# Performance work log

Hardware: AMD Instinct MI355X
Metric: run time of the kernel (lower is better)

The kernel has to match this reference:

```python
import jax, jax.numpy as jnp
import numpy as np

B, S, DIM = 2, 2048, 2048
H = 16
Q_LORA, KV_LORA = 512, 512
D_NOPE, D_ROPE, D_V = 128, 64, 128
D_QK = D_NOPE + D_ROPE  # 192
SCALE = D_QK ** -0.5
EPS = 1e-6


def rmsnorm(x, w):
    return x * jax.lax.rsqrt(jnp.mean(x * x, axis=-1, keepdims=True) + EPS) * w


def apply_rope(x, cos, sin):
    # x: [B, S, h, d] with d even; cos/sin: [S, d//2] (complex-pair rotation)
    xs = x.reshape(*x.shape[:-1], -1, 2)
    x0, x1 = xs[..., 0], xs[..., 1]
    c = cos[None, :, None, :]
    s = sin[None, :, None, :]
    out = jnp.stack([x0 * c - x1 * s, x0 * s + x1 * c], axis=-1)
    return out.reshape(x.shape)


def setup_inputs() -> dict:
    key = jax.random.key(0)
    ks = jax.random.split(key, 8)
    std = 0.02
    x = jax.random.normal(ks[0], (B, S, DIM), dtype=jnp.float32)
    wq_a_w = jax.random.normal(ks[1], (DIM, Q_LORA), dtype=jnp.float32) * std
    wq_a_b = jnp.zeros((Q_LORA,), dtype=jnp.float32)
    q_norm_w = jnp.ones((Q_LORA,), dtype=jnp.float32)
    wq_b_w = jax.random.normal(ks[2], (Q_LORA, H * D_QK), dtype=jnp.float32) * std
    wkv_a_w = jax.random.normal(ks[3], (DIM, KV_LORA + D_ROPE), dtype=jnp.float32) * std
    wkv_a_b = jnp.zeros((KV_LORA + D_ROPE,), dtype=jnp.float32)
    kv_norm_w = jnp.ones((KV_LORA,), dtype=jnp.float32)
    wkv_b_w = jax.random.normal(ks[4], (KV_LORA, H * (D_NOPE + D_V)), dtype=jnp.float32) * std
    wo_w = jax.random.normal(ks[5], (H * D_V, DIM), dtype=jnp.float32) * std
    # rotary table: freqs_cis[t, i] = exp(1j * t * 10000^{-2i/d})
    inv_freq = 1.0 / (10000.0 ** (np.arange(0, D_ROPE, 2, dtype=np.float32) / D_ROPE))
    t = np.arange(S, dtype=np.float32)
    ang = np.outer(t, inv_freq)  # [S, D_ROPE//2]
    freqs_cos = jnp.asarray(np.cos(ang), dtype=jnp.float32)
    freqs_sin = jnp.asarray(np.sin(ang), dtype=jnp.float32)
    # causal mask (prefill): 0 on/below diagonal, -1e9 above
    mask = jnp.where(jnp.arange(S)[:, None] >= jnp.arange(S)[None, :], 0.0, -1e9).astype(jnp.float32)
    return {"x": x, "wq_a_w": wq_a_w, "wq_a_b": wq_a_b, "q_norm_w": q_norm_w,
            "wq_b_w": wq_b_w, "wkv_a_w": wkv_a_w, "wkv_a_b": wkv_a_b,
            "kv_norm_w": kv_norm_w, "wkv_b_w": wkv_b_w, "wo_w": wo_w,
            "freqs_cos": freqs_cos, "freqs_sin": freqs_sin, "mask": mask,
            "start_pos": 0}


def reference(x, wq_a_w, wq_a_b, q_norm_w, wq_b_w, wkv_a_w, wkv_a_b,
              kv_norm_w, wkv_b_w, wo_w, freqs_cos, freqs_sin, mask, start_pos):
    bsz, seqlen, _ = x.shape
    # low-rank Q: wq_b(q_norm(wq_a(x)))
    q = rmsnorm(x @ wq_a_w + wq_a_b, q_norm_w) @ wq_b_w
    q = q.reshape(bsz, seqlen, H, D_QK)
    q_nope, q_pe = q[..., :D_NOPE], q[..., D_NOPE:]
    q_pe = apply_rope(q_pe, freqs_cos, freqs_sin)
    # low-rank KV
    kv_full = x @ wkv_a_w + wkv_a_b
    kv, k_pe = kv_full[..., :KV_LORA], kv_full[..., KV_LORA:]
    k_pe = apply_rope(k_pe[:, :, None, :], freqs_cos, freqs_sin)  # [B,S,1,D_ROPE]
    kv = rmsnorm(kv, kv_norm_w) @ wkv_b_w
    kv = kv.reshape(bsz, seqlen, H, D_NOPE + D_V)
    k_nope, v = kv[..., :D_NOPE], kv[..., D_NOPE:]
    k = jnp.concatenate([k_nope, jnp.broadcast_to(k_pe, (bsz, seqlen, H, D_ROPE))], axis=-1)
    # prefill (start_pos=0): cache[:, :end_pos] == freshly written k, v
    q = jnp.concatenate([q_nope, q_pe], axis=-1)
    scores = jnp.einsum('bshd,bthd->bsht', q, k) * SCALE
    scores = scores + mask[None, :, None, :]
    attn = jax.nn.softmax(scores.astype(jnp.float32), axis=-1).astype(q.dtype)
    out = jnp.einsum('bsht,bthd->bshd', attn, v)
    return out.reshape(bsz, seqlen, H * D_V) @ wo_w
```

## Files before the change

### kernel.cpp

```cpp
#include <hip/hip_runtime.h>
#include <hip/hip_bf16.h>

typedef unsigned short u16;
typedef unsigned int u32;
typedef __attribute__((ext_vector_type(8))) __bf16 bf16x8;
typedef __attribute__((ext_vector_type(4))) float f32x4;
typedef __attribute__((ext_vector_type(4))) u32 u32x4;
typedef __attribute__((ext_vector_type(2))) u32 u32x2;

#define S_LEN 2048
#define BF16_ONE 0x3F80u

__device__ __forceinline__ float b2f(u16 u) {
  union { unsigned u; float f; } v; v.u = ((unsigned)u) << 16; return v.f;
}
__device__ __forceinline__ u16 f2b(float f) {
  union { float f; unsigned u; } v; v.f = f;
  unsigned r = v.u + 0x7fffu + ((v.u >> 16) & 1u);
  return (u16)(r >> 16);
}
__device__ __forceinline__ u32 cvt_pk_bf16(float a, float b) {
  u32 r;
  asm("v_cvt_pk_bf16_f32 %0, %1, %2" : "=v"(r) : "v"(a), "v"(b));
  return r;
}

__device__ __forceinline__ void glds16(const u16* g, u16* l) {
  __builtin_amdgcn_global_load_lds((const __attribute__((address_space(1))) void*)g,
                                   (__attribute__((address_space(3))) void*)l, 16, 0, 0);
}

__device__ __forceinline__ bool probe_f32(const u16* p) { return p[0] != (u16)BF16_ONE; }

struct CvtDesc {
  const void* src[7];
  u16* dst[7];
  int cum[8];
};
__global__ __launch_bounds__(256) void cvt_batch(CvtDesc d, const u16* __restrict__ probe,
                                                 int total) {
  int i = blockIdx.x * 256 + threadIdx.x;
  if (i >= total) return;
  int t = 0;
#pragma unroll
  for (int k = 1; k < 7; ++k) t += (i >= d.cum[k]);
  int li = i - d.cum[t];
  if (probe_f32(probe)) {
    const float* s = (const float*)d.src[t] + (long)li * 8;
    u16 tmp[8];
#pragma unroll
    for (int j = 0; j < 8; ++j) tmp[j] = f2b(s[j]);
    *(u32x4*)(d.dst[t] + (long)li * 8) = *(const u32x4*)tmp;
  } else {
    *(u32x4*)(d.dst[t] + (long)li * 8) = ((const u32x4*)d.src[t])[li];
  }
}

struct TrDesc {
  const void* in[5];
  u16* out[5];
  int R[5], C[5];
  int tcum[6];
  float scale[5];
};
__global__ __launch_bounds__(256) void transpose_batch(TrDesc d,
                                                       const u16* __restrict__ probe) {
  __shared__ u16 tile[32][33];
  int bid = blockIdx.x;
  int t = 0;
#pragma unroll
  for (int k = 1; k < 5; ++k) t += (bid >= d.tcum[k]);
  int rem = bid - d.tcum[t];
  const int R = d.R[t], C = d.C[t];
  const int tilesX = C >> 5;
  const int bx = rem % tilesX, by = rem / tilesX;
  const int c0 = bx * 32, r0 = by * 32;
  const int tx = threadIdx.x, ty = threadIdx.y;
  const float sc = d.scale[t];
  if (probe_f32(probe)) {
    const float* inf = (const float*)d.in[t];
#pragma unroll
    for (int i = 0; i < 4; ++i)
      tile[ty + i * 8][tx] = f2b(inf[(long)(r0 + ty + i * 8) * C + c0 + tx] * sc);
  } else {
    const u16* inb = (const u16*)d.in[t];
#pragma unroll
    for (int i = 0; i < 4; ++i)
      tile[ty + i * 8][tx] = f2b(b2f(inb[(long)(r0 + ty + i * 8) * C + c0 + tx]) * sc);
  }
  __syncthreads();
  u16* outp = d.out[t];
#pragma unroll
  for (int i = 0; i < 4; ++i)
    outp[(long)(c0 + ty + i * 8) * R + r0 + tx] = tile[tx][ty + i * 8];
}

__global__ __launch_bounds__(256) void transpose_v(const u16* __restrict__ kvb,
                                                   u16* __restrict__ vt) {
  __shared__ u16 tile[32][33];
  int s0 = blockIdx.x * 32, d0 = blockIdx.y * 32, bh = blockIdx.z;
  int b = bh >> 4, h = bh & 15;
  int tx = threadIdx.x, ty = threadIdx.y;
#pragma unroll
  for (int i = 0; i < 4; ++i)
    tile[ty + i * 8][tx] =
        kvb[((long)b * S_LEN + s0 + ty + i * 8) * 4096 + h * 256 + 128 + d0 + tx];
  __syncthreads();
#pragma unroll
  for (int i = 0; i < 4; ++i)
    vt[((long)bh * 128 + d0 + ty + i * 8) * S_LEN + s0 + tx] = tile[tx][ty + i * 8];
}

template <int MT>
__global__ __launch_bounds__(256) void gemm_bt(const u16* __restrict__ A,
                                               const u16* __restrict__ Bt,
                                               const u16* __restrict__ bias,
                                               void* __restrict__ Cv,
                                               int M, int N, int K,
                                               const u16* __restrict__ oprobe) {
  constexpr int MI = MT / 32;
  __shared__ u16 As[2][MT * 32];
  __shared__ u16 Bs[2][128 * 32];
  const int tid = threadIdx.x;
  const int lane = tid & 63;
  const int w = tid >> 6;
  const int quad = lane >> 4;
  const int l16 = lane & 15;
  const int m0 = blockIdx.y * MT;
  const int n0 = blockIdx.x * 128;
  const int wm = (w >> 1) * (MT / 2);
  const int wn = (w & 1) * 64;

  const f32x4 zero = {0.f, 0.f, 0.f, 0.f};
  f32x4 acc[MI][4];
#pragma unroll
  for (int i = 0; i < MI; ++i)
#pragma unroll
    for (int j = 0; j < 4; ++j) acc[i][j] = zero;

  auto stage = [&](int k0, int buf) {
#pragma unroll
    for (int cc = 0; cc < MT * 4; cc += 256) {
      int j = cc + tid, ar = j >> 2, ak = ((j & 3) ^ (ar & 3)) * 8;
      glds16(A + (long)(m0 + ar) * K + k0 + ak, As[buf] + j * 8);
    }
#pragma unroll
    for (int cc = 0; cc < 512; cc += 256) {
      int j = cc + tid, br = j >> 2, bk = ((j & 3) ^ (br & 3)) * 8;
      int bn = n0 + br; if (bn > N - 1) bn = N - 1;
      glds16(Bt + (long)bn * K + k0 + bk, Bs[buf] + j * 8);
    }
  };

  const int nk = K >> 5;
  stage(0, 0);
  for (int t = 0; t < nk; ++t) {
    __syncthreads();
    if (t + 1 < nk) stage((t + 1) << 5, (t + 1) & 1);
    const u16* as = As[t & 1];
    const u16* bs = Bs[t & 1];
    bf16x8 af[MI], bfr[4];
#pragma unroll
    for (int mi = 0; mi < MI; ++mi)
      af[mi] = *(const bf16x8*)(as + (wm + mi * 16 + l16) * 32 +
                                ((quad ^ (l16 & 3)) * 8));
#pragma unroll
    for (int ni = 0; ni < 4; ++ni)
      bfr[ni] = *(const bf16x8*)(bs + (wn + ni * 16 + l16) * 32 +
                                 ((quad ^ (l16 & 3)) * 8));
#pragma unroll
    for (int mi = 0; mi < MI; ++mi)
#pragma unroll
      for (int ni = 0; ni < 4; ++ni)
        acc[mi][ni] = __builtin_amdgcn_mfma_f32_16x16x32_bf16(af[mi], bfr[ni],
                                                              acc[mi][ni], 0, 0, 0);
  }

  u16* C = (u16*)Cv;
  float* Cf = (float*)Cv;
  const bool of32 = oprobe && probe_f32(oprobe);
#pragma unroll
  for (int ni = 0; ni < 4; ++ni) {
    int col = n0 + wn + ni * 16 + l16;
    if (col >= N) continue;
    float bv = bias ? b2f(bias[col]) : 0.0f;
#pragma unroll
    for (int mi = 0; mi < MI; ++mi) {
      int row = m0 + wm + mi * 16 + quad * 4;
#pragma unroll
      for (int r = 0; r < 4; ++r) {
        float val = acc[mi][ni][r] + bv;
        if (of32) Cf[(long)(row + r) * N + col] = val;
        else      C[(long)(row + r) * N + col] = f2b(val);
      }
    }
  }
}

__global__ __launch_bounds__(256) void rmsnorm512(const u16* __restrict__ in, int in_stride,
                                                  const u16* __restrict__ w,
                                                  u16* __restrict__ out, int out_stride) {
  __shared__ float red[4];
  int row = blockIdx.x, tid = threadIdx.x;
  const u16* x = in + (long)row * in_stride;
  float v0 = b2f(x[tid]), v1 = b2f(x[tid + 256]);
  float ss = v0 * v0 + v1 * v1;
#pragma unroll
  for (int off = 1; off < 64; off <<= 1) ss += __shfl_xor(ss, off);
  if ((tid & 63) == 0) red[tid >> 6] = ss;
  __syncthreads();
  float tot = red[0] + red[1] + red[2] + red[3];
  float r = rsqrtf(tot * (1.0f / 512.0f) + 1e-6f);
  u16* y = out + (long)row * out_stride;
  y[tid] = f2b(v0 * r * b2f(w[tid]));
  y[tid + 256] = f2b(v1 * r * b2f(w[tid + 256]));
}

__global__ __launch_bounds__(256) void rope_q_kernel(u16* __restrict__ q,
                                                     const u16* __restrict__ fc,
                                                     const u16* __restrict__ fs) {
  int i = blockIdx.x * 256 + threadIdx.x;
  int pair = i & 31;
  int h = (i >> 5) & 15;
  int row = i >> 9;
  int pos = row & (S_LEN - 1);
  long base = (long)row * 3072 + h * 192 + 128 + pair * 2;
  float x0 = b2f(q[base]), x1 = b2f(q[base + 1]);
  float c = b2f(fc[pos * 32 + pair]), s = b2f(fs[pos * 32 + pair]);
  q[base] = f2b(x0 * c - x1 * s);
  q[base + 1] = f2b(x0 * s + x1 * c);
}

__global__ __launch_bounds__(256) void rope_k_kernel(const u16* __restrict__ qkva,
                                                     u16* __restrict__ kpe,
                                                     const u16* __restrict__ fc,
                                                     const u16* __restrict__ fs) {
  int i = blockIdx.x * 256 + threadIdx.x;
  int pair = i & 31;
  int row = i >> 5;
  int pos = row & (S_LEN - 1);
  long sb = (long)row * 1088 + 1024 + pair * 2;
  float x0 = b2f(qkva[sb]), x1 = b2f(qkva[sb + 1]);
  float c = b2f(fc[pos * 32 + pair]), s = b2f(fs[pos * 32 + pair]);
  kpe[(long)row * 64 + pair * 2] = f2b(x0 * c - x1 * s);
  kpe[(long)row * 64 + pair * 2 + 1] = f2b(x0 * s + x1 * c);
}

__global__ __launch_bounds__(512, 1) void mla_attn(const u16* __restrict__ q,
                                                   const u16* __restrict__ kvb,
                                                   const u16* __restrict__ vt,
                                                   const u16* __restrict__ kpe,
                                                   u16* __restrict__ o) {
  __shared__ u16 Ks[2][2][64 * 192];
  __shared__ u16 Vts[2][128 * 64];
  const int tid = threadIdx.x;
  const int w = tid >> 6;
  const int g = w >> 2;
  const int sw = w & 3;
  const int lane = tid & 63;
  const int quad = lane >> 4;
  const int l16 = lane & 15;
  const int bh = blockIdx.x;
  const int b = bh >> 4, h = bh & 15;
  const long rowbase = (long)b * S_LEN;
  const f32x4 zero = {0.f, 0.f, 0.f, 0.f};

  auto stage_k = [&](int t0s, u16* dst) {
#pragma unroll
    for (int tt = 0; tt < 3; ++tt) {
      int j = tt * 512 + tid;
      int r = j / 24, csw = j % 24;
      int c = csw ^ (r & 7);
      const u16* src = (c < 16)
                           ? (kvb + (rowbase + t0s + r) * 4096 + h * 256 + c * 8)
                           : (kpe + (rowbase + t0s + r) * 64 + (c - 16) * 8);
      glds16(src, dst + j * 8);
    }
  };
  auto stage_v = [&](int t0s, u16* dst) {
#pragma unroll
    for (int tt = 0; tt < 2; ++tt) {
      int j = tt * 512 + tid;
      int d = j >> 3, c = (j & 7) ^ (d & 7);
      glds16(vt + ((long)bh * 128 + d) * S_LEN + t0s + c * 8, dst + j * 8);
    }
  };

  const int srcA = (((quad & 1) << 1) | (quad >> 1)) * 16 + l16;
  const int srcB = srcA ^ 16;
  const bool lowq = quad < 2;
  const int p = quad & 1;

  const int yy = blockIdx.y;
  const int jt = (yy < 8) ? yy : 23 - yy;
  const int q0 = jt * 128;
  const int ns = jt + 1;
  const int rowlo = q0 + sw * 32;

  const u16* qrowA = q + (rowbase + rowlo + l16) * 3072 + h * 192;
  const u16* qrowB = qrowA + 16 * 3072;
  bf16x8 qfA[6], qfB[6];
#pragma unroll
  for (int kk = 0; kk < 6; ++kk) {
    qfA[kk] = *(const bf16x8*)(qrowA + kk * 32 + quad * 8);
    qfB[kk] = *(const bf16x8*)(qrowB + kk * 32 + quad * 8);
  }

  float mA = -INFINITY, mB = -INFINITY;
  float lA = 0.f, lB = 0.f;
  f32x4 oA[8], oB[8];
#pragma unroll
  for (int i = 0; i < 8; ++i) { oA[i] = zero; oB[i] = zero; }

  auto finish_half = [&](f32x4* s, float& m_r, float& l_r, f32x4* oacc,
                         int lim, bool needmask, bf16x8& ap0, bf16x8& ap1) {
    if (needmask) {
#pragma unroll
      for (int gg = 0; gg < 4; ++gg)
#pragma unroll
        for (int r = 0; r < 4; ++r)
          s[gg][r] = (gg * 16 + r > lim) ? -1e30f : s[gg][r];
    }
    float mx0 = fmaxf(fmaxf(s[0][0], s[0][1]), fmaxf(s[0][2], s[0][3]));
    float mx1 = fmaxf(fmaxf(s[1][0], s[1][1]), fmaxf(s[1][2], s[1][3]));
    float mx2 = fmaxf(fmaxf(s[2][0], s[2][1]), fmaxf(s[2][2], s[2][3]));
    float mx3 = fmaxf(fmaxf(s[3][0], s[3][1]), fmaxf(s[3][2], s[3][3]));
    float vmax = fmaxf(fmaxf(mx0, mx1), fmaxf(mx2, mx3));
    vmax = fmaxf(vmax, __shfl_xor(vmax, 16));
    vmax = fmaxf(vmax, __shfl_xor(vmax, 32));

    if (!__all(vmax <= m_r + 8.0f)) {
      float mnew = fmaxf(m_r, vmax);
      float alpha = __expf(m_r - mnew);
      m_r = mnew;
      l_r *= alpha;
      float al0 = __shfl(alpha, (lane & 48) | (quad * 4 + 0));
      float al1 = __shfl(alpha, (lane & 48) | (quad * 4 + 1));
      float al2 = __shfl(alpha, (lane & 48) | (quad * 4 + 2));
      float al3 = __shfl(alpha, (lane & 48) | (quad * 4 + 3));
#pragma unroll
      for (int nt = 0; nt < 8; ++nt) {
        f32x4 tt = oacc[nt];
        tt[0] *= al0; tt[1] *= al1; tt[2] *= al2; tt[3] *= al3;
        oacc[nt] = tt;
      }
    }

    float e00 = __expf(s[0][0] - m_r), e01 = __expf(s[0][1] - m_r);
    float e02 = __expf(s[0][2] - m_r), e03 = __expf(s[0][3] - m_r);
    float e10 = __expf(s[1][0] - m_r), e11 = __expf(s[1][1] - m_r);
    float e12 = __expf(s[1][2] - m_r), e13 = __expf(s[1][3] - m_r);
    float e20 = __expf(s[2][0] - m_r), e21 = __expf(s[2][1] - m_r);
    float e22 = __expf(s[2][2] - m_r), e23 = __expf(s[2][3] - m_r);
    float e30 = __expf(s[3][0] - m_r), e31 = __expf(s[3][1] - m_r);
    float e32 = __expf(s[3][2] - m_r), e33 = __expf(s[3][3] - m_r);
    l_r += ((e00 + e01) + (e02 + e03)) + ((e10 + e11) + (e12 + e13)) +
           ((e20 + e21) + (e22 + e23)) + ((e30 + e31) + (e32 + e33));
    u32 pk0x = cvt_pk_bf16(e00, e01), pk0y = cvt_pk_bf16(e02, e03);
    u32 pk1x = cvt_pk_bf16(e10, e11), pk1y = cvt_pk_bf16(e12, e13);
    u32 pk2x = cvt_pk_bf16(e20, e21), pk2y = cvt_pk_bf16(e22, e23);
    u32 pk3x = cvt_pk_bf16(e30, e31), pk3y = cvt_pk_bf16(e32, e33);

    u32 a0c = p ? pk1x : pk0x, a1c = p ? pk1y : pk0y;
    u32 a2c = p ? pk3x : pk2x, a3c = p ? pk3y : pk2y;
    u32 b0c = p ? pk0x : pk1x, b1c = p ? pk0y : pk1y;
    u32 b2c = p ? pk2x : pk3x, b3c = p ? pk2y : pk3y;
    u32 A0 = __shfl(a0c, srcA), A1 = __shfl(a1c, srcA);
    u32 A2 = __shfl(a2c, srcA), A3 = __shfl(a3c, srcA);
    u32 B0 = __shfl(b0c, srcB), B1 = __shfl(b1c, srcB);
    u32 B2 = __shfl(b2c, srcB), B3 = __shfl(b3c, srcB);
    u32x4 w0 = {lowq ? A0 : B0, lowq ? A1 : B1, lowq ? B0 : A0, lowq ? B1 : A1};
    u32x4 w1 = {lowq ? A2 : B2, lowq ? A3 : B3, lowq ? B2 : A2, lowq ? B3 : A3};
    ap0 = __builtin_bit_cast(bf16x8, w0);
    ap1 = __builtin_bit_cast(bf16x8, w1);
  };

  stage_k(0, Ks[0][0]);
  stage_k(64, Ks[0][1]);

  for (int i = 0; i < ns; ++i) {
    __syncthreads();
    stage_v((2 * i) * 64, Vts[0]);
    stage_v((2 * i + 1) * 64, Vts[1]);
    if (i + 1 < ns) {
      stage_k((2 * i + 2) * 64, Ks[(i + 1) & 1][0]);
      stage_k((2 * i + 3) * 64, Ks[(i + 1) & 1][1]);
    }
    const int t0 = (2 * i + g) * 64;
    const bool active = (rowlo + 31 >= t0);
    bf16x8 apA0, apA1, apB0, apB1;
    if (active) {
      const u16* ks = Ks[i & 1][g];
      f32x4 sA[4] = {zero, zero, zero, zero};
      f32x4 sB[4] = {zero, zero, zero, zero};
      __builtin_amdgcn_s_setprio(1);
#pragma unroll
      for (int kk = 0; kk < 6; ++kk) {
        const int csw = ((kk * 4 + quad) ^ (l16 & 7)) * 8;
#pragma unroll
        for (int gg = 0; gg < 4; ++gg) {
          bf16x8 kf = *(const bf16x8*)(ks + (gg * 16 + l16) * 192 + csw);
          sA[gg] = __builtin_amdgcn_mfma_f32_16x16x32_bf16(kf, qfA[kk], sA[gg], 0, 0, 0);
          sB[gg] = __builtin_amdgcn_mfma_f32_16x16x32_bf16(kf, qfB[kk], sB[gg], 0, 0, 0);
        }
      }
      __builtin_amdgcn_s_setprio(0);

      const bool nmA = (t0 + 63 > rowlo);
      const bool nmB = (t0 + 63 > rowlo + 16);
      const int limA = rowlo + l16 - t0 - quad * 4;
      finish_half(sA, mA, lA, oA, limA, nmA, apA0, apA1);
      finish_half(sB, mB, lB, oB, limA + 16, nmB, apB0, apB1);
    }
    __syncthreads();
    if (active) {
      const u16* vs = Vts[g];
      __builtin_amdgcn_s_setprio(1);
#pragma unroll
      for (int nt = 0; nt < 8; ++nt) {
        bf16x8 bv0 = *(const bf16x8*)(vs + (nt * 16 + l16) * 64 +
                                      ((quad ^ (l16 & 7)) * 8));
        bf16x8 bv1 = *(const bf16x8*)(vs + (nt * 16 + l16) * 64 +
                                      (((4 + quad) ^ (l16 & 7)) * 8));
        oA[nt] = __builtin_amdgcn_mfma_f32_16x16x32_bf16(apA0, bv0, oA[nt], 0, 0, 0);
        oA[nt] = __builtin_amdgcn_mfma_f32_16x16x32_bf16(apA1, bv1, oA[nt], 0, 0, 0);
        oB[nt] = __builtin_amdgcn_mfma_f32_16x16x32_bf16(apB0, bv0, oB[nt], 0, 0, 0);
        oB[nt] = __builtin_amdgcn_mfma_f32_16x16x32_bf16(apB1, bv1, oB[nt], 0, 0, 0);
      }
      __builtin_amdgcn_s_setprio(0);
    }
  }

  float lsA = lA; lsA += __shfl_xor(lsA, 16); lsA += __shfl_xor(lsA, 32);
  float lsB = lB; lsB += __shfl_xor(lsB, 16); lsB += __shfl_xor(lsB, 32);

  float* zone = (float*)&Ks[0][0][0];
  float* mlz = zone + 16384;
  if (g == 1) {
    float* zp0 = zone + ((sw * 2 + 0) * 64 + lane) * 32;
    float* zp1 = zone + ((sw * 2 + 1) * 64 + lane) * 32;
#pragma unroll
    for (int nt = 0; nt < 8; ++nt) {
      *(f32x4*)(zp0 + ((nt ^ (lane & 7)) << 2)) = oA[nt];
      *(f32x4*)(zp1 + ((nt ^ (lane & 7)) << 2)) = oB[nt];
    }
    mlz[((sw * 2 + 0) * 64 + lane) * 2 + 0] = mA;
    mlz[((sw * 2 + 0) * 64 + lane) * 2 + 1] = lsA;
    mlz[((sw * 2 + 1) * 64 + lane) * 2 + 0] = mB;
    mlz[((sw * 2 + 1) * 64 + lane) * 2 + 1] = lsB;
  }
  __syncthreads();
  if (g == 0) {
    auto merge_write = [&](float m_r, float ls, f32x4* oacc, int hz) {
      const float* zp = zone + ((sw * 2 + hz) * 64 + lane) * 32;
      float mo = mlz[((sw * 2 + hz) * 64 + lane) * 2 + 0];
      float lo = mlz[((sw * 2 + hz) * 64 + lane) * 2 + 1];
      float mm = fmaxf(m_r, mo);
      float aA = __expf(m_r - mm);
      float aB = __expf(mo - mm);
      float lt = ls * aA + lo * aB;
      float sAl = __fdividef(aA, lt);
      float sBl = __fdividef(aB, lt);
      float sa[4], sb[4];
#pragma unroll
      for (int r = 0; r < 4; ++r) {
        int src = (lane & 48) | (quad * 4 + r);
        sa[r] = __shfl(sAl, src);
        sb[r] = __shfl(sBl, src);
      }
      const long orow = rowbase + q0 + sw * 32 + hz * 16 + quad * 4;
#pragma unroll
      for (int nt = 0; nt < 8; ++nt) {
        f32x4 op = *(const f32x4*)(zp + ((nt ^ (lane & 7)) << 2));
#pragma unroll
        for (int r = 0; r < 4; ++r)
          o[(orow + r) * 2048 + h * 128 + nt * 16 + l16] =
              f2b(oacc[nt][r] * sa[r] + op[r] * sb[r]);
      }
    };
    merge_write(mA, lsA, oA, 0);
    merge_write(mB, lsB, oB, 1);
  }
}

extern "C" void kernel_launch(void* const* d_in, const int* in_sizes, int n_in,
                              void* d_out, int out_size, void* d_ws, size_t ws_size,
                              hipStream_t stream) {
  const void* x_raw    = d_in[0];
  const void* wqa_raw  = d_in[1];
  const void* wqab_raw = d_in[2];
  const void* qnw_raw  = d_in[3];
  const void* wqb_raw  = d_in[4];
  const void* wkva_raw = d_in[5];
  const void* wkvab_raw= d_in[6];
  const void* kvnw_raw = d_in[7];
  const void* wkvb_raw = d_in[8];
  const void* wo_raw   = d_in[9];
  const void* fc_raw   = d_in[10];
  const void* fs_raw   = d_in[11];
  const u16* probe = (const u16*)qnw_raw;
  const float SC = 0.07216878364870323f;

  char* ws = (char*)d_ws;
  size_t off = 0;
  auto alloc = [&](size_t n) { void* p = ws + off; off += (n + 255) & ~(size_t)255; return p; };
  u16* xb     = (u16*)alloc(4096ull * 2048 * 2);
  u16* fcb    = (u16*)alloc(2048ull * 32 * 2);
  u16* fsb    = (u16*)alloc(2048ull * 32 * 2);
  u16* biasc  = (u16*)alloc(1088ull * 2);
  u16* qnw_b  = (u16*)alloc(512ull * 2);
  u16* kvnw_b = (u16*)alloc(512ull * 2);
  u16* qkvat  = (u16*)alloc(1088ull * 2048 * 2);
  u16* wqb_t  = (u16*)alloc(3072ull * 512 * 2);
  u16* wkvb_t = (u16*)alloc(4096ull * 512 * 2);
  u16* wo_t   = (u16*)alloc(2048ull * 2048 * 2);
  u16* qkva   = (u16*)alloc(4096ull * 1088 * 2);
  u16* qa     = (u16*)alloc(4096ull * 512 * 2);
  u16* qbuf   = (u16*)alloc(4096ull * 3072 * 2);
  u16* kvn    = (u16*)alloc(4096ull * 512 * 2);
  u16* kpe    = (u16*)alloc(4096ull * 64 * 2);
  u16* kvb    = (u16*)alloc(4096ull * 4096 * 2);
  u16* vtb    = (u16*)alloc(32ull * 128 * 2048 * 2);
  u16* attn   = (u16*)alloc(4096ull * 2048 * 2);

  CvtDesc cd;
  const void* csrc[7] = {x_raw, fc_raw, fs_raw, wqab_raw, qnw_raw, wkvab_raw, kvnw_raw};
  u16* cdst[7] = {xb, fcb, fsb, biasc, qnw_b, biasc + 512, kvnw_b};
  long cn[7] = {4096l * 2048, 2048l * 32, 2048l * 32, 512, 512, 576, 512};
  int cum = 0;
  for (int i = 0; i < 7; ++i) {
    cd.src[i] = csrc[i]; cd.dst[i] = cdst[i];
    cd.cum[i] = cum; cum += (int)(cn[i] / 8);
  }
  cd.cum[7] = cum;
  cvt_batch<<<(cum + 255) / 256, 256, 0, stream>>>(cd, probe, cum);

  TrDesc td;
  const void* tin[5] = {wqa_raw, wqb_raw, wkva_raw, wkvb_raw, wo_raw};
  u16* tout[5] = {qkvat, wqb_t, qkvat + 512ull * 2048, wkvb_t, wo_t};
  int tR[5] = {2048, 512, 2048, 512, 2048};
  int tC[5] = {512, 3072, 576, 4096, 2048};
  float tsc[5] = {1.0f, SC, 1.0f, 1.0f, 1.0f};
  int tcum = 0;
  for (int i = 0; i < 5; ++i) {
    td.in[i] = tin[i]; td.out[i] = tout[i];
    td.R[i] = tR[i]; td.C[i] = tC[i]; td.scale[i] = tsc[i];
    td.tcum[i] = tcum; tcum += (tR[i] / 32) * (tC[i] / 32);
  }
  td.tcum[5] = tcum;
  transpose_batch<<<tcum, dim3(32, 8), 0, stream>>>(td, probe);

  gemm_bt<128><<<dim3(9, 32), 256, 0, stream>>>(xb, qkvat, biasc, qkva, 4096, 1088, 2048, nullptr);

  rmsnorm512<<<4096, 256, 0, stream>>>(qkva, 1088, qnw_b, qa, 512);
  gemm_bt<128><<<dim3(24, 32), 256, 0, stream>>>(qa, wqb_t, nullptr, qbuf, 4096, 3072, 512, nullptr);
  rope_q_kernel<<<8192, 256, 0, stream>>>(qbuf, fcb, fsb);

  rmsnorm512<<<4096, 256, 0, stream>>>(qkva + 512, 1088, kvnw_b, kvn, 512);
  rope_k_kernel<<<512, 256, 0, stream>>>(qkva, kpe, fcb, fsb);
  gemm_bt<128><<<dim3(32, 32), 256, 0, stream>>>(kvn, wkvb_t, nullptr, kvb, 4096, 4096, 512, nullptr);
  transpose_v<<<dim3(64, 4, 32), dim3(32, 8), 0, stream>>>(kvb, vtb);

  mla_attn<<<dim3(32, 16), 512, 0, stream>>>(qbuf, kvb, vtb, kpe, attn);

  gemm_bt<128><<<dim3(16, 32), 256, 0, stream>>>(attn, wo_t, nullptr, d_out, 4096, 2048, 2048, probe);
}
```

Measured before the change: 403.0 us.

## Fuse V transpose into kv GEMM epilogue and merge norm/rope launches

```diff
diff --git a/kernel.cpp b/kernel.cpp
--- a/kernel.cpp
+++ b/kernel.cpp
@@ -95,29 +95,14 @@
     outp[(long)(c0 + ty + i * 8) * R + r0 + tx] = tile[tx][ty + i * 8];
 }
 
-__global__ __launch_bounds__(256) void transpose_v(const u16* __restrict__ kvb,
-                                                   u16* __restrict__ vt) {
-  __shared__ u16 tile[32][33];
-  int s0 = blockIdx.x * 32, d0 = blockIdx.y * 32, bh = blockIdx.z;
-  int b = bh >> 4, h = bh & 15;
-  int tx = threadIdx.x, ty = threadIdx.y;
-#pragma unroll
-  for (int i = 0; i < 4; ++i)
-    tile[ty + i * 8][tx] =
-        kvb[((long)b * S_LEN + s0 + ty + i * 8) * 4096 + h * 256 + 128 + d0 + tx];
-  __syncthreads();
-#pragma unroll
-  for (int i = 0; i < 4; ++i)
-    vt[((long)bh * 128 + d0 + ty + i * 8) * S_LEN + s0 + tx] = tile[tx][ty + i * 8];
-}
-
 template <int MT>
 __global__ __launch_bounds__(256) void gemm_bt(const u16* __restrict__ A,
                                                const u16* __restrict__ Bt,
                                                const u16* __restrict__ bias,
                                                void* __restrict__ Cv,
                                                int M, int N, int K,
-                                               const u16* __restrict__ oprobe) {
+                                               const u16* __restrict__ oprobe,
+                                               u16* __restrict__ vtOut) {
   constexpr int MI = MT / 32;
   __shared__ u16 As[2][MT * 32];
   __shared__ u16 Bs[2][128 * 32];
@@ -184,25 +169,43 @@
     int col = n0 + wn + ni * 16 + l16;
     if (col >= N) continue;
     float bv = bias ? b2f(bias[col]) : 0.0f;
+    const int lc = col & 255;
+    const bool toV = (vtOut != nullptr) && (lc >= 128);
 #pragma unroll
     for (int mi = 0; mi < MI; ++mi) {
       int row = m0 + wm + mi * 16 + quad * 4;
-#pragma unroll
-      for (int r = 0; r < 4; ++r) {
-        float val = acc[mi][ni][r] + bv;
-        if (of32) Cf[(long)(row + r) * N + col] = val;
-        else      C[(long)(row + r) * N + col] = f2b(val);
+      if (toV) {
+        int hh = col >> 8, d = lc - 128;
+        int bb = row >> 11, s = row & 2047;
+        u32 lo = (u32)f2b(acc[mi][ni][0] + bv) | ((u32)f2b(acc[mi][ni][1] + bv) << 16);
+        u32 hi = (u32)f2b(acc[mi][ni][2] + bv) | ((u32)f2b(acc[mi][ni][3] + bv) << 16);
+        u32x2 pk = {lo, hi};
+        *(u32x2*)(vtOut + ((long)(bb * 16 + hh) * 128 + d) * 2048 + s) = pk;
+      } else {
+#pragma unroll
+        for (int r = 0; r < 4; ++r) {
+          float val = acc[mi][ni][r] + bv;
+          if (of32) Cf[(long)(row + r) * N + col] = val;
+          else      C[(long)(row + r) * N + col] = f2b(val);
+        }
       }
     }
   }
 }
 
-__global__ __launch_bounds__(256) void rmsnorm512(const u16* __restrict__ in, int in_stride,
-                                                  const u16* __restrict__ w,
-                                                  u16* __restrict__ out, int out_stride) {
+__global__ __launch_bounds__(256) void rmsnorm_dual(const u16* __restrict__ qkva,
+                                                    const u16* __restrict__ qw,
+                                                    const u16* __restrict__ kw,
+                                                    u16* __restrict__ qa,
+                                                    u16* __restrict__ kvn) {
   __shared__ float red[4];
-  int row = blockIdx.x, tid = threadIdx.x;
-  const u16* x = in + (long)row * in_stride;
+  const int bid = blockIdx.x;
+  const bool kv = bid >= 4096;
+  const int row = kv ? bid - 4096 : bid;
+  const int tid = threadIdx.x;
+  const u16* x = qkva + (long)row * 1088 + (kv ? 512 : 0);
+  const u16* w = kv ? kw : qw;
+  u16* y = (kv ? kvn : qa) + (long)row * 512;
   float v0 = b2f(x[tid]), v1 = b2f(x[tid + 256]);
   float ss = v0 * v0 + v1 * v1;
 #pragma unroll
@@ -211,39 +214,38 @@
   __syncthreads();
   float tot = red[0] + red[1] + red[2] + red[3];
   float r = rsqrtf(tot * (1.0f / 512.0f) + 1e-6f);
-  u16* y = out + (long)row * out_stride;
   y[tid] = f2b(v0 * r * b2f(w[tid]));
   y[tid + 256] = f2b(v1 * r * b2f(w[tid + 256]));
 }
 
-__global__ __launch_bounds__(256) void rope_q_kernel(u16* __restrict__ q,
-                                                     const u16* __restrict__ fc,
-                                                     const u16* __restrict__ fs) {
-  int i = blockIdx.x * 256 + threadIdx.x;
-  int pair = i & 31;
-  int h = (i >> 5) & 15;
-  int row = i >> 9;
-  int pos = row & (S_LEN - 1);
-  long base = (long)row * 3072 + h * 192 + 128 + pair * 2;
-  float x0 = b2f(q[base]), x1 = b2f(q[base + 1]);
-  float c = b2f(fc[pos * 32 + pair]), s = b2f(fs[pos * 32 + pair]);
-  q[base] = f2b(x0 * c - x1 * s);
-  q[base + 1] = f2b(x0 * s + x1 * c);
-}
-
-__global__ __launch_bounds__(256) void rope_k_kernel(const u16* __restrict__ qkva,
-                                                     u16* __restrict__ kpe,
-                                                     const u16* __restrict__ fc,
-                                                     const u16* __restrict__ fs) {
-  int i = blockIdx.x * 256 + threadIdx.x;
-  int pair = i & 31;
-  int row = i >> 5;
-  int pos = row & (S_LEN - 1);
-  long sb = (long)row * 1088 + 1024 + pair * 2;
-  float x0 = b2f(qkva[sb]), x1 = b2f(qkva[sb + 1]);
-  float c = b2f(fc[pos * 32 + pair]), s = b2f(fs[pos * 32 + pair]);
-  kpe[(long)row * 64 + pair * 2] = f2b(x0 * c - x1 * s);
-  kpe[(long)row * 64 + pair * 2 + 1] = f2b(x0 * s + x1 * c);
+__global__ __launch_bounds__(256) void rope_all(u16* __restrict__ q,
+                                                const u16* __restrict__ qkva,
+                                                u16* __restrict__ kpe,
+                                                const u16* __restrict__ fc,
+                                                const u16* __restrict__ fs) {
+  const int bid = blockIdx.x;
+  if (bid < 8192) {
+    int i = bid * 256 + threadIdx.x;
+    int pair = i & 31;
+    int h = (i >> 5) & 15;
+    int row = i >> 9;
+    int pos = row & (S_LEN - 1);
+    long base = (long)row * 3072 + h * 192 + 128 + pair * 2;
+    float x0 = b2f(q[base]), x1 = b2f(q[base + 1]);
+    float c = b2f(fc[pos * 32 + pair]), s = b2f(fs[pos * 32 + pair]);
+    q[base] = f2b(x0 * c - x1 * s);
+    q[base + 1] = f2b(x0 * s + x1 * c);
+  } else {
+    int i = (bid - 8192) * 256 + threadIdx.x;
+    int pair = i & 31;
+    int row = i >> 5;
+    int pos = row & (S_LEN - 1);
+    long sb = (long)row * 1088 + 1024 + pair * 2;
+    float x0 = b2f(qkva[sb]), x1 = b2f(qkva[sb + 1]);
+    float c = b2f(fc[pos * 32 + pair]), s = b2f(fs[pos * 32 + pair]);
+    kpe[(long)row * 64 + pair * 2] = f2b(x0 * c - x1 * s);
+    kpe[(long)row * 64 + pair * 2 + 1] = f2b(x0 * s + x1 * c);
+  }
 }
 
 __global__ __launch_bounds__(512, 1) void mla_attn(const u16* __restrict__ q,
@@ -550,18 +552,17 @@
   td.tcum[5] = tcum;
   transpose_batch<<<tcum, dim3(32, 8), 0, stream>>>(td, probe);
 
-  gemm_bt<128><<<dim3(9, 32), 256, 0, stream>>>(xb, qkvat, biasc, qkva, 4096, 1088, 2048, nullptr);
-
-  rmsnorm512<<<4096, 256, 0, stream>>>(qkva, 1088, qnw_b, qa, 512);
-  gemm_bt<128><<<dim3(24, 32), 256, 0, stream>>>(qa, wqb_t, nullptr, qbuf, 4096, 3072, 512, nullptr);
-  rope_q_kernel<<<8192, 256, 0, stream>>>(qbuf, fcb, fsb);
-
-  rmsnorm512<<<4096, 256, 0, stream>>>(qkva + 512, 1088, kvnw_b, kvn, 512);
-  rope_k_kernel<<<512, 256, 0, stream>>>(qkva, kpe, fcb, fsb);
-  gemm_bt<128><<<dim3(32, 32), 256, 0, stream>>>(kvn, wkvb_t, nullptr, kvb, 4096, 4096, 512, nullptr);
-  transpose_v<<<dim3(64, 4, 32), dim3(32, 8), 0, stream>>>(kvb, vtb);
+  gemm_bt<128><<<dim3(9, 32), 256, 0, stream>>>(xb, qkvat, biasc, qkva, 4096, 1088, 2048, nullptr, nullptr);
+
+  rmsnorm_dual<<<8192, 256, 0, stream>>>(qkva, qnw_b, kvnw_b, qa, kvn);
+
+  gemm_bt<128><<<dim3(24, 32), 256, 0, stream>>>(qa, wqb_t, nullptr, qbuf, 4096, 3072, 512, nullptr, nullptr);
+
+  rope_all<<<8704, 256, 0, stream>>>(qbuf, qkva, kpe, fcb, fsb);
+
+  gemm_bt<128><<<dim3(32, 32), 256, 0, stream>>>(kvn, wkvb_t, nullptr, kvb, 4096, 4096, 512, nullptr, vtb);
 
   mla_attn<<<dim3(32, 16), 512, 0, stream>>>(qbuf, kvb, vtb, kpe, attn);
 
-  gemm_bt<128><<<dim3(16, 32), 256, 0, stream>>>(attn, wo_t, nullptr, d_out, 4096, 2048, 2048, probe);
-}
+  gemm_bt<128><<<dim3(16, 32), 256, 0, stream>>>(attn, wo_t, nullptr, d_out, 4096, 2048, 2048, probe, nullptr);
+}
```

Result: faster. 389.0 us (-3.5%).
